# Kernel optimization log

Hardware: AMD Instinct MI355X
Metric: run time of the kernel (lower is better)

## Reference

```python
import jax, jax.numpy as jnp
import numpy as np

B = 4096
D_IN = 2048
D_H = 2048
W_SCALE = 0.02  # keep exp() gate pre-activations small / numerically safe


def setup_inputs() -> dict:
    key = jax.random.key(0)
    ks = jax.random.split(key, 16)
    inp = {
        "x": jax.random.normal(ks[0], (B, D_IN), jnp.float32),
        "h_prev": jax.random.normal(ks[1], (B, D_H), jnp.float32),
        "c_prev": jax.random.normal(ks[2], (B, D_H), jnp.float32),
        "n_prev": jax.random.uniform(ks[3], (B, D_H), jnp.float32),
    }
    # input->hidden weights (stored [in, out]; torch Linear computes x @ W.T + b,
    # equivalent to x @ W_here + b) and biases
    for i, name in enumerate(["i", "f", "o", "z"]):
        inp[f"W_{name}"] = jax.random.normal(ks[4 + i], (D_IN, D_H), jnp.float32) * W_SCALE
        inp[f"b_{name}"] = jax.random.normal(ks[8 + i], (D_H,), jnp.float32) * W_SCALE
        inp[f"U_{name}"] = jax.random.normal(ks[12 + i], (D_H, D_H), jnp.float32) * W_SCALE
    return inp


def reference(x, h_prev, c_prev, n_prev,
              W_i, b_i, U_i, W_f, b_f, U_f,
              W_o, b_o, U_o, W_z, b_z, U_z):
    # Gate pre-activations: 8 GEMMs fused pairwise per gate
    i = jnp.exp(x @ W_i + b_i + h_prev @ U_i)
    f = jnp.exp(x @ W_f + b_f + h_prev @ U_f)
    o = jax.nn.sigmoid(x @ W_o + b_o + h_prev @ U_o)
    z = jnp.tanh(x @ W_z + b_z + h_prev @ U_z)
    c = f * c_prev + i * z
    n = f * n_prev + i
    h = o * (c / (n + 1e-6))
    return (h, c, n)
```

## Files before the change

### kernel.cpp

```cpp
#include <hip/hip_runtime.h>
#include <hip/hip_bf16.h>
#include <stdint.h>

#define B_DIM 4096
#define DH    2048
#define K_DIM 4096
#define N_DIM 8192

typedef __bf16  bf16x8 __attribute__((ext_vector_type(8)));
typedef float   f32x4  __attribute__((ext_vector_type(4)));

__device__ __forceinline__ unsigned short f2bf(float f) {
  unsigned int u = __float_as_uint(f);
  u += 0x7FFFu + ((u >> 16) & 1u);
  return (unsigned short)(u >> 16);
}

__global__ void cast_cat_A(const float* __restrict__ x, const float* __restrict__ h,
                           unsigned short* __restrict__ Abuf) {
  int idx = blockIdx.x * 256 + threadIdx.x;
  const int half = B_DIM * (DH / 4);
  bool isx = (idx < half);
  int i2 = isx ? idx : idx - half;
  int b  = i2 >> 9;
  int c4 = i2 & 511;
  const float* src = (isx ? x : h) + (((size_t)b) << 11) + (c4 << 2);
  float4 v = *(const float4*)src;
  ushort4 o;
  o.x = f2bf(v.x); o.y = f2bf(v.y); o.z = f2bf(v.z); o.w = f2bf(v.w);
  int col = (isx ? 0 : DH) + (c4 << 2);
  *(ushort4*)(Abuf + (size_t)b * K_DIM + col) = o;
}

__global__ void transpose_cast_B(const float* __restrict__ Wi, const float* __restrict__ Ui,
                                 const float* __restrict__ Wf, const float* __restrict__ Uf,
                                 const float* __restrict__ Wo, const float* __restrict__ Uo,
                                 const float* __restrict__ Wz, const float* __restrict__ Uz,
                                 unsigned short* __restrict__ Bt) {
  __shared__ unsigned short lds[64 * 68];
  const int k0 = blockIdx.x * 64;
  const int g  = blockIdx.y >> 5;
  const int j0 = (blockIdx.y & 31) * 64;
  const float* W = (g == 0) ? Wi : (g == 1) ? Wf : (g == 2) ? Wo : Wz;
  const float* U = (g == 0) ? Ui : (g == 1) ? Uf : (g == 2) ? Uo : Uz;
  const float* src = ((k0 < DH) ? (W + (size_t)k0 * DH)
                                : (U + (size_t)(k0 - DH) * DH)) + j0;
  const int t = threadIdx.x;
  #pragma unroll
  for (int r = 0; r < 4; ++r) {
    int slot = r * 256 + t;
    int kk = slot >> 4;
    int c4 = slot & 15;
    float4 v = *(const float4*)(src + (size_t)kk * DH + (c4 << 2));
    int n = c4 << 2;
    lds[(n + 0) * 68 + kk] = f2bf(v.x);
    lds[(n + 1) * 68 + kk] = f2bf(v.y);
    lds[(n + 2) * 68 + kk] = f2bf(v.z);
    lds[(n + 3) * 68 + kk] = f2bf(v.w);
  }
  __syncthreads();
  #pragma unroll
  for (int r = 0; r < 4; ++r) {
    int slot = r * 256 + t;
    int nn = slot >> 4;
    int c8 = slot & 15;
    int j  = j0 + nn;
    int np = ((j >> 5) << 7) + ((j & 16) << 2) + (g << 4) + (j & 15);
    *(ushort4*)(Bt + (size_t)np * K_DIM + k0 + (c8 << 2)) =
        *(const ushort4*)(lds + nn * 68 + (c8 << 2));
  }
}

__global__ __launch_bounds__(256, 3) void gemm_gates(const unsigned short* __restrict__ A,
                                                     const unsigned short* __restrict__ Bt,
                                                     const float* __restrict__ bi, const float* __restrict__ bf,
                                                     const float* __restrict__ bo, const float* __restrict__ bz,
                                                     const float* __restrict__ cprev, const float* __restrict__ nprev,
                                                     float* __restrict__ out) {
  __shared__ alignas(16) unsigned short As[128 * 32];
  __shared__ alignas(16) unsigned short Bs[128 * 32];
  const int t    = threadIdx.x;
  const int wave = t >> 6;
  const int lane = t & 63;
  const int m0 = blockIdx.y * 128;
  const int n0 = blockIdx.x * 128;
  const int wm = (wave & 1) * 64;
  const int wn = (wave >> 1) * 64;
  const int lm = lane & 15;
  const int kg = lane >> 4;

  f32x4 acc[4][4] = {};

  const int c0 = t, c1 = t + 256;
  const unsigned short* pa0 = A  + (size_t)(m0 + (c0 >> 2)) * K_DIM + (c0 & 3) * 8;
  const unsigned short* pa1 = A  + (size_t)(m0 + (c1 >> 2)) * K_DIM + (c1 & 3) * 8;
  const unsigned short* pb0 = Bt + (size_t)(n0 + (c0 >> 2)) * K_DIM + (c0 & 3) * 8;
  const unsigned short* pb1 = Bt + (size_t)(n0 + (c1 >> 2)) * K_DIM + (c1 & 3) * 8;
  unsigned short* lA0 = As + (wave * 64) * 8;
  unsigned short* lA1 = As + (256 + wave * 64) * 8;
  unsigned short* lB0 = Bs + (wave * 64) * 8;
  unsigned short* lB1 = Bs + (256 + wave * 64) * 8;

  const int aoff = (wm + lm) * 32 + kg * 8;
  const int boff = (wn + lm) * 32 + kg * 8;

  for (int k0 = 0; k0 < K_DIM; k0 += 32) {
    __builtin_amdgcn_global_load_lds((const __attribute__((address_space(1))) unsigned int*)(pa0 + k0),
                                     (__attribute__((address_space(3))) unsigned int*)lA0, 16, 0, 0);
    __builtin_amdgcn_global_load_lds((const __attribute__((address_space(1))) unsigned int*)(pa1 + k0),
                                     (__attribute__((address_space(3))) unsigned int*)lA1, 16, 0, 0);
    __builtin_amdgcn_global_load_lds((const __attribute__((address_space(1))) unsigned int*)(pb0 + k0),
                                     (__attribute__((address_space(3))) unsigned int*)lB0, 16, 0, 0);
    __builtin_amdgcn_global_load_lds((const __attribute__((address_space(1))) unsigned int*)(pb1 + k0),
                                     (__attribute__((address_space(3))) unsigned int*)lB1, 16, 0, 0);
    __syncthreads();
    bf16x8 av[4], bv[4];
    #pragma unroll
    for (int mi = 0; mi < 4; ++mi)
      av[mi] = *(const bf16x8*)(As + aoff + mi * 16 * 32);
    #pragma unroll
    for (int ni = 0; ni < 4; ++ni)
      bv[ni] = *(const bf16x8*)(Bs + boff + ni * 16 * 32);
    #pragma unroll
    for (int mi = 0; mi < 4; ++mi) {
      #pragma unroll
      for (int ni = 0; ni < 4; ++ni)
        acc[mi][ni] = __builtin_amdgcn_mfma_f32_16x16x32_bf16(av[mi], bv[ni], acc[mi][ni], 0, 0, 0);
    }
    __syncthreads();
  }

  const int jj = (blockIdx.x << 5) + ((wn >> 6) << 4) + lm;
  const float vbi = bi[jj], vbf = bf[jj], vbo = bo[jj], vbz = bz[jj];
  #pragma unroll
  for (int mi = 0; mi < 4; ++mi) {
    const int mrow = m0 + wm + mi * 16 + kg * 4;
    #pragma unroll
    for (int r = 0; r < 4; ++r) {
      const size_t idx = (size_t)(mrow + r) * DH + jj;
      float pi = acc[mi][0][r] + vbi;
      float pf = acc[mi][1][r] + vbf;
      float po = acc[mi][2][r] + vbo;
      float pz = acc[mi][3][r] + vbz;
      float iv = __expf(pi);
      float fv = __expf(pf);
      float ov = 1.0f / (1.0f + __expf(-po));
      float t2 = __expf(2.0f * pz);
      float zv = 1.0f - 2.0f / (t2 + 1.0f);
      float cv = fv * cprev[idx] + iv * zv;
      float nv = fv * nprev[idx] + iv;
      out[idx]            = ov * (cv / (nv + 1e-6f));
      out[8388608 + idx]  = cv;
      out[16777216 + idx] = nv;
    }
  }
}

extern "C" void kernel_launch(void* const* d_in, const int* in_sizes, int n_in,
                              void* d_out, int out_size, void* d_ws, size_t ws_size,
                              hipStream_t stream) {
  const float* x      = (const float*)d_in[0];
  const float* h_prev = (const float*)d_in[1];
  const float* c_prev = (const float*)d_in[2];
  const float* n_prev = (const float*)d_in[3];
  const float* W_i = (const float*)d_in[4];  const float* b_i = (const float*)d_in[5];  const float* U_i = (const float*)d_in[6];
  const float* W_f = (const float*)d_in[7];  const float* b_f = (const float*)d_in[8];  const float* U_f = (const float*)d_in[9];
  const float* W_o = (const float*)d_in[10]; const float* b_o = (const float*)d_in[11]; const float* U_o = (const float*)d_in[12];
  const float* W_z = (const float*)d_in[13]; const float* b_z = (const float*)d_in[14]; const float* U_z = (const float*)d_in[15];
  float* out = (float*)d_out;

  char* ws = (char*)d_ws;
  unsigned short* Abuf = (unsigned short*)ws;
  unsigned short* Bt   = (unsigned short*)(ws + 33554432);

  cast_cat_A<<<16384, 256, 0, stream>>>(x, h_prev, Abuf);
  transpose_cast_B<<<dim3(64, 128), 256, 0, stream>>>(W_i, U_i, W_f, U_f, W_o, U_o, W_z, U_z, Bt);
  gemm_gates<<<dim3(64, 32), 256, 0, stream>>>(Abuf, Bt, b_i, b_f, b_o, b_z, c_prev, n_prev, out);
}
```

Before: 627.3 us.

## Rewrite gate GEMM with 256x256 tiles, 4-stage LDS pipeline, swizzle

The gate GEMM moves from 128x128 tiles with 256 threads to 256x256 tiles with 512 threads. Global-to-LDS loads now go through a 4-deep ring of buffers, with explicit vmcnt waits and a single barrier per k-step, replacing the load-sync-compute-sync loop. An XOR swizzle on LDS columns reduces bank conflicts, blocks are remapped for L2 locality, and s_setprio raises priority around the MFMA bursts. The goal is to hide memory latency and raise data reuse, at the cost of 128KB of LDS per block and more accumulator registers, which lowers occupancy.

Result: faster. 557.5 us (-11.1%).

```diff
diff --git a/kernel.cpp b/kernel.cpp
--- a/kernel.cpp
+++ b/kernel.cpp
@@ -6,6 +6,7 @@
 #define DH    2048
 #define K_DIM 4096
 #define N_DIM 8192
+#define NT    128
 
 typedef __bf16  bf16x8 __attribute__((ext_vector_type(8)));
 typedef float   f32x4  __attribute__((ext_vector_type(4)));
@@ -71,70 +72,111 @@
   }
 }
 
-__global__ __launch_bounds__(256, 3) void gemm_gates(const unsigned short* __restrict__ A,
+__global__ __launch_bounds__(512, 2) void gemm_gates(const unsigned short* __restrict__ A,
                                                      const unsigned short* __restrict__ Bt,
                                                      const float* __restrict__ bi, const float* __restrict__ bf,
                                                      const float* __restrict__ bo, const float* __restrict__ bz,
                                                      const float* __restrict__ cprev, const float* __restrict__ nprev,
                                                      float* __restrict__ out) {
-  __shared__ alignas(16) unsigned short As[128 * 32];
-  __shared__ alignas(16) unsigned short Bs[128 * 32];
+  __shared__ alignas(16) unsigned short lds[65536];
+  unsigned short* As = lds;
+  unsigned short* Bs = lds + 32768;
+
   const int t    = threadIdx.x;
-  const int wave = t >> 6;
+  const int w    = t >> 6;
   const int lane = t & 63;
-  const int m0 = blockIdx.y * 128;
-  const int n0 = blockIdx.x * 128;
-  const int wm = (wave & 1) * 64;
-  const int wn = (wave >> 1) * 64;
-  const int lm = lane & 15;
-  const int kg = lane >> 4;
-
-  f32x4 acc[4][4] = {};
-
-  const int c0 = t, c1 = t + 256;
-  const unsigned short* pa0 = A  + (size_t)(m0 + (c0 >> 2)) * K_DIM + (c0 & 3) * 8;
-  const unsigned short* pa1 = A  + (size_t)(m0 + (c1 >> 2)) * K_DIM + (c1 & 3) * 8;
-  const unsigned short* pb0 = Bt + (size_t)(n0 + (c0 >> 2)) * K_DIM + (c0 & 3) * 8;
-  const unsigned short* pb1 = Bt + (size_t)(n0 + (c1 >> 2)) * K_DIM + (c1 & 3) * 8;
-  unsigned short* lA0 = As + (wave * 64) * 8;
-  unsigned short* lA1 = As + (256 + wave * 64) * 8;
-  unsigned short* lB0 = Bs + (wave * 64) * 8;
-  unsigned short* lB1 = Bs + (256 + wave * 64) * 8;
-
-  const int aoff = (wm + lm) * 32 + kg * 8;
-  const int boff = (wn + lm) * 32 + kg * 8;
-
-  for (int k0 = 0; k0 < K_DIM; k0 += 32) {
-    __builtin_amdgcn_global_load_lds((const __attribute__((address_space(1))) unsigned int*)(pa0 + k0),
-                                     (__attribute__((address_space(3))) unsigned int*)lA0, 16, 0, 0);
-    __builtin_amdgcn_global_load_lds((const __attribute__((address_space(1))) unsigned int*)(pa1 + k0),
-                                     (__attribute__((address_space(3))) unsigned int*)lA1, 16, 0, 0);
-    __builtin_amdgcn_global_load_lds((const __attribute__((address_space(1))) unsigned int*)(pb0 + k0),
-                                     (__attribute__((address_space(3))) unsigned int*)lB0, 16, 0, 0);
-    __builtin_amdgcn_global_load_lds((const __attribute__((address_space(1))) unsigned int*)(pb1 + k0),
-                                     (__attribute__((address_space(3))) unsigned int*)lB1, 16, 0, 0);
-    __syncthreads();
+  const int lm   = lane & 15;
+  const int kg   = lane >> 4;
+  const int wm   = w >> 2;
+  const int wn   = w & 3;
+
+  const int flat = blockIdx.y * 32 + blockIdx.x;
+  const int swzb = (flat & 7) * 64 + (flat >> 3);
+  const int bx   = swzb & 31;
+  const int by   = swzb >> 5;
+  const int m0   = by * 256;
+  const int n0   = bx * 256;
+
+  const int r4 = lane >> 2, c4 = lane & 3;
+  const int rowS0 = w * 32 + r4;
+  const int rowS1 = rowS0 + 16;
+  const int kby0 = (c4 * 16) ^ (((rowS0 >> 1) & 3) << 4);
+  const int kby1 = (c4 * 16) ^ (((rowS1 >> 1) & 3) << 4);
+  const unsigned short* pa0 = A  + (size_t)(m0 + rowS0) * K_DIM + (kby0 >> 1);
+  const unsigned short* pa1 = A  + (size_t)(m0 + rowS1) * K_DIM + (kby1 >> 1);
+  const unsigned short* pb0 = Bt + (size_t)(n0 + rowS0) * K_DIM + (kby0 >> 1);
+  const unsigned short* pb1 = Bt + (size_t)(n0 + rowS1) * K_DIM + (kby1 >> 1);
+  const int ldsQ0 = (w * 32) * 32;
+  const int ldsQ1 = (w * 32 + 16) * 32;
+
+  const int aoff = (wm * 128 + lm) * 64 + ((kg * 16) ^ (((lm >> 1) & 3) << 4));
+  const int boff = (wn * 64  + lm) * 64 + ((kg * 16) ^ (((lm >> 1) & 3) << 4));
+  const char* Asc = (const char*)As;
+  const char* Bsc = (const char*)Bs;
+
+  f32x4 acc[8][4] = {};
+
+#define STAGE(tile) do {                                                                              \
+    const int _buf = (tile) & 3;                                                                      \
+    const size_t _k = (size_t)(tile) * 32;                                                            \
+    __builtin_amdgcn_global_load_lds((const __attribute__((address_space(1))) unsigned int*)(pa0 + _k), \
+        (__attribute__((address_space(3))) unsigned int*)(As + _buf * 8192 + ldsQ0), 16, 0, 0);       \
+    __builtin_amdgcn_global_load_lds((const __attribute__((address_space(1))) unsigned int*)(pa1 + _k), \
+        (__attribute__((address_space(3))) unsigned int*)(As + _buf * 8192 + ldsQ1), 16, 0, 0);       \
+    __builtin_amdgcn_global_load_lds((const __attribute__((address_space(1))) unsigned int*)(pb0 + _k), \
+        (__attribute__((address_space(3))) unsigned int*)(Bs + _buf * 8192 + ldsQ0), 16, 0, 0);       \
+    __builtin_amdgcn_global_load_lds((const __attribute__((address_space(1))) unsigned int*)(pb1 + _k), \
+        (__attribute__((address_space(3))) unsigned int*)(Bs + _buf * 8192 + ldsQ1), 16, 0, 0);       \
+  } while (0)
+
+  STAGE(0); STAGE(1); STAGE(2);
+  asm volatile("s_waitcnt vmcnt(8)" ::: "memory");
+  __builtin_amdgcn_s_barrier();
+  asm volatile("" ::: "memory");
+
+  for (int kt = 0; kt < NT; ++kt) {
+    const int cur = kt & 3;
+    if (kt + 3 < NT) STAGE(kt + 3);
+
+    const char* ab = Asc + cur * 16384 + aoff;
+    const char* bb = Bsc + cur * 16384 + boff;
+
     bf16x8 av[4], bv[4];
     #pragma unroll
-    for (int mi = 0; mi < 4; ++mi)
-      av[mi] = *(const bf16x8*)(As + aoff + mi * 16 * 32);
-    #pragma unroll
-    for (int ni = 0; ni < 4; ++ni)
-      bv[ni] = *(const bf16x8*)(Bs + boff + ni * 16 * 32);
-    #pragma unroll
-    for (int mi = 0; mi < 4; ++mi) {
+    for (int ni = 0; ni < 4; ++ni) bv[ni] = *(const bf16x8*)(bb + ni * 1024);
+
+    #pragma unroll
+    for (int i = 0; i < 4; ++i) av[i] = *(const bf16x8*)(ab + i * 1024);
+    __builtin_amdgcn_s_setprio(1);
+    #pragma unroll
+    for (int i = 0; i < 4; ++i)
       #pragma unroll
       for (int ni = 0; ni < 4; ++ni)
-        acc[mi][ni] = __builtin_amdgcn_mfma_f32_16x16x32_bf16(av[mi], bv[ni], acc[mi][ni], 0, 0, 0);
-    }
-    __syncthreads();
-  }
-
-  const int jj = (blockIdx.x << 5) + ((wn >> 6) << 4) + lm;
+        acc[i][ni] = __builtin_amdgcn_mfma_f32_16x16x32_bf16(av[i], bv[ni], acc[i][ni], 0, 0, 0);
+    __builtin_amdgcn_s_setprio(0);
+
+    #pragma unroll
+    for (int i = 0; i < 4; ++i) av[i] = *(const bf16x8*)(ab + 4096 + i * 1024);
+    __builtin_amdgcn_s_setprio(1);
+    #pragma unroll
+    for (int i = 0; i < 4; ++i)
+      #pragma unroll
+      for (int ni = 0; ni < 4; ++ni)
+        acc[4 + i][ni] = __builtin_amdgcn_mfma_f32_16x16x32_bf16(av[i], bv[ni], acc[4 + i][ni], 0, 0, 0);
+    __builtin_amdgcn_s_setprio(0);
+
+    if (kt + 3 < NT)      asm volatile("s_waitcnt vmcnt(8)" ::: "memory");
+    else if (kt + 2 < NT) asm volatile("s_waitcnt vmcnt(4)" ::: "memory");
+    else                  asm volatile("s_waitcnt vmcnt(0)" ::: "memory");
+    __builtin_amdgcn_s_barrier();
+    asm volatile("" ::: "memory");
+  }
+
+  const int jj = bx * 64 + (wn >> 1) * 32 + (wn & 1) * 16 + lm;
   const float vbi = bi[jj], vbf = bf[jj], vbo = bo[jj], vbz = bz[jj];
   #pragma unroll
-  for (int mi = 0; mi < 4; ++mi) {
-    const int mrow = m0 + wm + mi * 16 + kg * 4;
+  for (int mi = 0; mi < 8; ++mi) {
+    const int mrow = m0 + wm * 128 + mi * 16 + kg * 4;
     #pragma unroll
     for (int r = 0; r < 4; ++r) {
       const size_t idx = (size_t)(mrow + r) * DH + jj;
@@ -154,6 +196,7 @@
       out[16777216 + idx] = nv;
     }
   }
+#undef STAGE
 }
 
 extern "C" void kernel_launch(void* const* d_in, const int* in_sizes, int n_in,
@@ -175,5 +218,5 @@
 
   cast_cat_A<<<16384, 256, 0, stream>>>(x, h_prev, Abuf);
   transpose_cast_B<<<dim3(64, 128), 256, 0, stream>>>(W_i, U_i, W_f, U_f, W_o, U_o, W_z, U_z, Bt);
-  gemm_gates<<<dim3(64, 32), 256, 0, stream>>>(Abuf, Bt, b_i, b_f, b_o, b_z, c_prev, n_prev, out);
-}
+  gemm_gates<<<dim3(32, 16), 512, 0, stream>>>(Abuf, Bt, b_i, b_f, b_o, b_z, c_prev, n_prev, out);
+}
```
